# Optimization experiments

Hardware: AMD Instinct MI355X
Metric: run time of the kernel (lower is better)

Reference implementation:

```python
import jax, jax.numpy as jnp
import numpy as np

B, S, E, L = 4, 4096, 1024, 64
SCALE = float(np.sqrt(L))


def setup_inputs() -> dict:
    key = jax.random.key(0)
    ks = jax.random.split(key, 7)
    x = jax.random.normal(ks[0], (B, S, E), dtype=jnp.float32)
    # causal mask: positions with mask==0 are disallowed (masked_fill semantics)
    mask = jnp.tril(jnp.ones((S, S), dtype=jnp.int32))
    # Linear params (torch Linear: y = x @ W.T + b); store as [E, L] for x @ W
    sd = 1.0 / np.sqrt(E)
    Wq = jax.random.uniform(ks[1], (E, L), jnp.float32, -sd, sd)
    Wk = jax.random.uniform(ks[2], (E, L), jnp.float32, -sd, sd)
    Wv = jax.random.uniform(ks[3], (E, L), jnp.float32, -sd, sd)
    bq = jax.random.uniform(ks[4], (L,), jnp.float32, -sd, sd)
    bk = jax.random.uniform(ks[5], (L,), jnp.float32, -sd, sd)
    bv = jax.random.uniform(ks[6], (L,), jnp.float32, -sd, sd)
    return {"x": x, "Wq": Wq, "Wk": Wk, "Wv": Wv,
            "bq": bq, "bk": bk, "bv": bv, "mask": mask}


def reference(x, Wq, Wk, Wv, bq, bk, bv, mask):
    # Q,K,V: [B, S, L]
    Q = x @ Wq + bq
    K = x @ Wk + bk
    V = x @ Wv + bv
    # scores: [B, S, S] -- naive full matrix, faithful to the original
    scores = jnp.einsum('bsl,btl->bst', Q, K) / SCALE
    scores = jnp.where(mask == 0, -jnp.inf, scores)
    attn = jax.nn.softmax(scores, axis=-1)
    return jnp.einsum('bst,btl->bsl', attn, V)
```

## Files before the change

kernel.cpp:

```cpp
#include <hip/hip_runtime.h>
#include <hip/hip_bf16.h>
#include <cstdint>

typedef __bf16 bf16_t;
typedef __bf16 bf16x8 __attribute__((ext_vector_type(8)));
typedef float f32x4 __attribute__((ext_vector_type(4)));

#define B_ 4
#define S_ 4096
#define E_ 1024
#define L_ 64

__device__ __forceinline__ f32x4 mfma16(bf16x8 a, bf16x8 b, f32x4 c) {
  return __builtin_amdgcn_mfma_f32_16x16x32_bf16(a, b, c, 0, 0, 0);
}

template <int CTRL>
__device__ __forceinline__ float dpp_max_step(float x) {
  int t = __builtin_amdgcn_update_dpp(0, __float_as_int(x), CTRL, 0xF, 0xF, true);
  return fmaxf(x, __int_as_float(t));
}
template <int CTRL>
__device__ __forceinline__ float dpp_add_step(float x) {
  int t = __builtin_amdgcn_update_dpp(0, __float_as_int(x), CTRL, 0xF, 0xF, true);
  return x + __int_as_float(t);
}
__device__ __forceinline__ float dpp_reduce_max16(float x) {
  x = dpp_max_step<0x121>(x);
  x = dpp_max_step<0x122>(x);
  x = dpp_max_step<0x124>(x);
  x = dpp_max_step<0x128>(x);
  return x;
}
__device__ __forceinline__ float dpp_reduce_add16(float x) {
  x = dpp_add_step<0x121>(x);
  x = dpp_add_step<0x122>(x);
  x = dpp_add_step<0x124>(x);
  x = dpp_add_step<0x128>(x);
  return x;
}


__global__ void prep_w_kernel(const float* __restrict__ Wq, const float* __restrict__ Wk,
                              const float* __restrict__ Wv, bf16_t* __restrict__ Wf) {
  int n = blockIdx.x;
  const float* W = (n < 64) ? Wq : (n < 128 ? Wk : Wv);
  int col = n & 63;
  int nt = n >> 4, lr = n & 15;
  for (int k = threadIdx.x; k < E_; k += blockDim.x) {
    int kt = k >> 5, lg = (k >> 3) & 3, e = k & 7;
    Wf[((size_t)((nt * 32 + kt) * 64 + lg * 16 + lr) << 3) + e] = (bf16_t)W[(size_t)k * L_ + col];
  }
}

__global__ __launch_bounds__(512) void qkv_proj_kernel(
    const float* __restrict__ x, const bf16_t* __restrict__ Wf,
    const float* __restrict__ bq, const float* __restrict__ bk, const float* __restrict__ bv,
    bf16_t* __restrict__ Qf, bf16_t* __restrict__ Kf, bf16_t* __restrict__ Vf) {
  __shared__ __align__(16) char smem[32 * 1032 * 2];
  bf16_t* xls = reinterpret_cast<bf16_t*>(smem);
  bf16_t* stc = reinterpret_cast<bf16_t*>(smem);

  const int tid = threadIdx.x;
  const int w = tid >> 6, l = tid & 63;
  const int lr = l & 15, lg = l >> 4;
  const int rowgrp = w & 1, colgrp = w >> 1;
  const int m0 = blockIdx.x * 32;

  {
    const float* xb = x + (size_t)m0 * E_;
#pragma unroll
    for (int i = 0; i < 8; ++i) {
      const int base = (i * 512 + tid) * 8;
      float4 u0 = *reinterpret_cast<const float4*>(xb + base);
      float4 u1 = *reinterpret_cast<const float4*>(xb + base + 4);
      bf16x8 pk;
      pk[0] = (bf16_t)u0.x; pk[1] = (bf16_t)u0.y; pk[2] = (bf16_t)u0.z; pk[3] = (bf16_t)u0.w;
      pk[4] = (bf16_t)u1.x; pk[5] = (bf16_t)u1.y; pk[6] = (bf16_t)u1.z; pk[7] = (bf16_t)u1.w;
      const int row = base >> 10, col = base & 1023;
      *reinterpret_cast<bf16x8*>(xls + row * 1032 + col) = pk;
    }
  }
  __syncthreads();

  f32x4 acc[3];
#pragma unroll
  for (int t = 0; t < 3; ++t) acc[t] = f32x4{0.f, 0.f, 0.f, 0.f};

  const bf16_t* xa = xls + (size_t)(rowgrp * 16 + lr) * 1032 + lg * 8;
#pragma unroll
  for (int kt = 0; kt < 32; ++kt) {
    bf16x8 a = *reinterpret_cast<const bf16x8*>(xa + kt * 32);
#pragma unroll
    for (int t = 0; t < 3; ++t) {
      const int nt = colgrp * 3 + t;
      bf16x8 b = *reinterpret_cast<const bf16x8*>(Wf + (((size_t)(nt * 32 + kt) * 64 + l) << 3));
      acc[t] = mfma16(a, b, acc[t]);
    }
  }
  __syncthreads();

#pragma unroll
  for (int t = 0; t < 3; ++t) {
    const int colb = colgrp * 48 + t * 16;
    const int col = colb + lr;
    const int mat = colb >> 6;
    const float* bias = (mat == 0) ? bq : (mat == 1 ? bk : bv);
    const float bb = bias[col & 63];
#pragma unroll
    for (int r = 0; r < 4; ++r) {
      const int row = rowgrp * 16 + lg * 4 + r;
      stc[row * 200 + col] = (bf16_t)(acc[t][r] + bb);
    }
  }
  __syncthreads();

  if (tid < 256) {
    const int rt = tid >> 7, ktq = (tid >> 6) & 1, lane = tid & 63;
    const int lgw = lane >> 4, lrw = lane & 15;
    const int rtg = (m0 >> 4) + rt;
    bf16x8 qv = *reinterpret_cast<const bf16x8*>(stc + (rt * 16 + lrw) * 200 + ktq * 32 + lgw * 8);
    *reinterpret_cast<bf16x8*>(Qf + (((size_t)(rtg * 2 + ktq) * 64 + lane) << 3)) = qv;
    bf16x8 kv = *reinterpret_cast<const bf16x8*>(stc + (rt * 16 + lrw) * 200 + 64 + ktq * 32 + lgw * 8);
    *reinterpret_cast<bf16x8*>(Kf + (((size_t)(rtg * 2 + ktq) * 64 + lane) << 3)) = kv;
  } else {
    const int t2 = tid - 256;
    const int vt = t2 >> 6, lane = t2 & 63;
    const int lgv = lane >> 4, lrv = lane & 15;
    const int colv = vt * 16 + lrv;
    bf16x8 vv;
#pragma unroll
    for (int e = 0; e < 8; ++e)
      vv[e] = stc[(lgv * 8 + e) * 200 + 128 + colv];
    const int batch = m0 >> 12;
    const int stg = (m0 & (S_ - 1)) >> 5;
    *reinterpret_cast<bf16x8*>(Vf + ((size_t)batch << 18) + (((size_t)(stg * 4 + vt) * 64 + lane) << 3)) = vv;
  }
}

__global__ __launch_bounds__(256) void attn_kernel(
    const bf16_t* __restrict__ Qf, const bf16_t* __restrict__ Kf,
    const bf16_t* __restrict__ Vf, float* __restrict__ Opart, float* __restrict__ mlpart) {
  __shared__ __align__(16) bf16_t p_lds[4][16 * 72];
  __shared__ bf16_t od_lds[3][16][68];
  __shared__ float ml_lds[3][16][2];

  const int c = threadIdx.x >> 6, l = threadIdx.x & 63;
  const int lr = l & 15, lg = l >> 4;
  const int u = blockIdx.x;
  const int batch = u & 3;
  const int strip = (u >> 2) & 3;
  const int h = (u >> 4) & 1;
  const int qt = 63 - (u >> 5);
  const int qsi = ((u >> 5) << 4) | (u & 15);
  const int qrow = qt * 64 + strip * 16;
  const size_t qbase = (size_t)batch * S_ + qrow;
  bf16_t* pw = p_lds[c];

  const int rtq = batch * 256 + qt * 4 + strip;
  bf16x8 qa0 = *reinterpret_cast<const bf16x8*>(Qf + (((size_t)(rtq * 2) * 64 + l) << 3));
  bf16x8 qa1 = *reinterpret_cast<const bf16x8*>(Qf + (((size_t)(rtq * 2 + 1) * 64 + l) << 3));
  const bf16_t* Vb = Vf + ((size_t)batch << 18);

  f32x4 o[4];
  float m[4], ssum[4];
#pragma unroll
  for (int rr = 0; rr < 4; ++rr) { o[rr] = f32x4{0.f, 0.f, 0.f, 0.f}; m[rr] = -1e30f; ssum[rr] = 0.f; }

  for (int kt = 2 * c + h; kt <= qt; kt += 8) {
    const int t0 = kt * 64;
    f32x4 st[4];
#pragma unroll
    for (int cf = 0; cf < 4; ++cf) st[cf] = f32x4{0.f, 0.f, 0.f, 0.f};
#pragma unroll
    for (int cf = 0; cf < 4; ++cf) {
      const int rtk = batch * 256 + kt * 4 + cf;
      bf16x8 b0 = *reinterpret_cast<const bf16x8*>(Kf + (((size_t)(rtk * 2) * 64 + l) << 3));
      bf16x8 b1 = *reinterpret_cast<const bf16x8*>(Kf + (((size_t)(rtk * 2 + 1) * 64 + l) << 3));
      st[cf] = mfma16(qa0, b0, st[cf]);
      st[cf] = mfma16(qa1, b1, st[cf]);
    }
    const bool diag = (kt == qt);
    float p[4][4];
#pragma unroll
    for (int rr = 0; rr < 4; ++rr) {
      const int qg = qrow + lg * 4 + rr;
      float rowmax = -1e30f;
#pragma unroll
      for (int cf = 0; cf < 4; ++cf) {
        float s = st[cf][rr] * 0.125f;
        if (diag && (t0 + cf * 16 + lr) > qg) s = -1e30f;
        p[cf][rr] = s;
        rowmax = fmaxf(rowmax, s);
      }
      rowmax = dpp_reduce_max16(rowmax);
      float mnew = fmaxf(m[rr], rowmax);
      float scale = __expf(m[rr] - mnew);
      float rs = 0.f;
#pragma unroll
      for (int cf = 0; cf < 4; ++cf) {
        float e = __expf(p[cf][rr] - mnew);
        p[cf][rr] = e;
        rs += e;
      }
      rs = dpp_reduce_add16(rs);
      ssum[rr] = ssum[rr] * scale + rs;
#pragma unroll
      for (int cf = 0; cf < 4; ++cf) o[cf][rr] *= scale;
      m[rr] = mnew;
    }
#pragma unroll
    for (int rr = 0; rr < 4; ++rr)
#pragma unroll
      for (int cf = 0; cf < 4; ++cf)
        pw[(lg * 4 + rr) * 72 + cf * 16 + lr] = (bf16_t)p[cf][rr];
    bf16x8 pa0 = *reinterpret_cast<const bf16x8*>(pw + lr * 72 + lg * 8);
    bf16x8 pa1 = *reinterpret_cast<const bf16x8*>(pw + lr * 72 + 32 + lg * 8);
    const int st0 = kt * 2;
#pragma unroll
    for (int cf = 0; cf < 4; ++cf) {
      bf16x8 v0 = *reinterpret_cast<const bf16x8*>(Vb + (((size_t)((st0 * 4 + cf) * 64 + l)) << 3));
      bf16x8 v1 = *reinterpret_cast<const bf16x8*>(Vb + (((size_t)(((st0 + 1) * 4 + cf) * 64 + l)) << 3));
      o[cf] = mfma16(pa0, v0, o[cf]);
      o[cf] = mfma16(pa1, v1, o[cf]);
    }
  }

  if (c > 0) {
    if (lr == 0) {
#pragma unroll
      for (int rr = 0; rr < 4; ++rr) {
        ml_lds[c - 1][lg * 4 + rr][0] = m[rr];
        ml_lds[c - 1][lg * 4 + rr][1] = ssum[rr];
      }
    }
#pragma unroll
    for (int cf = 0; cf < 4; ++cf)
#pragma unroll
      for (int rr = 0; rr < 4; ++rr)
        od_lds[c - 1][lg * 4 + rr][cf * 16 + lr] = (bf16_t)o[cf][rr];
  }
  __syncthreads();
  if (c == 0) {
    float* Op = Opart + (size_t)(h * 1024 + qsi) * 1024;
    float* mlp = mlpart + (size_t)(h * 1024 + qsi) * 32;
#pragma unroll
    for (int rr = 0; rr < 4; ++rr) {
      const int row = lg * 4 + rr;
      float M = m[rr];
      float mv[3];
#pragma unroll
      for (int cc = 0; cc < 3; ++cc) {
        mv[cc] = ml_lds[cc][row][0];
        M = fmaxf(M, mv[cc]);
      }
      float f0 = __expf(m[rr] - M);
      float Lsum = ssum[rr] * f0;
      float fc[3];
#pragma unroll
      for (int cc = 0; cc < 3; ++cc) {
        fc[cc] = __expf(mv[cc] - M);
        Lsum += ml_lds[cc][row][1] * fc[cc];
      }
      if (lr == 0) { mlp[row * 2] = M; mlp[row * 2 + 1] = Lsum; }
#pragma unroll
      for (int cf = 0; cf < 4; ++cf) {
        float val = o[cf][rr] * f0;
#pragma unroll
        for (int cc = 0; cc < 3; ++cc)
          val += (float)od_lds[cc][row][cf * 16 + lr] * fc[cc];
        Op[row * 64 + cf * 16 + lr] = val;
      }
    }
  }
}

__global__ __launch_bounds__(64) void combine_kernel(
    const float* __restrict__ Opart, const float* __restrict__ mlpart,
    float* __restrict__ out) {
  const int b = blockIdx.x;
  const int batch = b & 3, strip = (b >> 2) & 3, qt = 63 - (b >> 4);
  const int l = threadIdx.x;
  const int row = l >> 2, c0 = (l & 3) * 16;
  const float* ml0 = mlpart + ((size_t)(0 * 1024 + b) * 16 + row) * 2;
  const float* ml1 = mlpart + ((size_t)(1 * 1024 + b) * 16 + row) * 2;
  float m0 = ml0[0], l0 = ml0[1], m1 = ml1[0], l1 = ml1[1];
  float M = fmaxf(m0, m1);
  float f0 = __expf(m0 - M), f1 = __expf(m1 - M);
  float inv = 1.f / (l0 * f0 + l1 * f1);
  const float* O0 = Opart + (size_t)(0 * 1024 + b) * 1024 + row * 64 + c0;
  const float* O1 = Opart + (size_t)(1 * 1024 + b) * 1024 + row * 64 + c0;
  float* dst = out + ((size_t)batch * S_ + qt * 64 + strip * 16 + row) * L_ + c0;
#pragma unroll
  for (int j = 0; j < 4; ++j) {
    float4 a = reinterpret_cast<const float4*>(O0)[j];
    float4 bb = reinterpret_cast<const float4*>(O1)[j];
    float4 v;
    v.x = (a.x * f0 + bb.x * f1) * inv;
    v.y = (a.y * f0 + bb.y * f1) * inv;
    v.z = (a.z * f0 + bb.z * f1) * inv;
    v.w = (a.w * f0 + bb.w * f1) * inv;
    reinterpret_cast<float4*>(dst)[j] = v;
  }
}

extern "C" void kernel_launch(void* const* d_in, const int* in_sizes, int n_in,
                              void* d_out, int out_size, void* d_ws, size_t ws_size,
                              hipStream_t stream) {
  (void)in_sizes; (void)n_in; (void)out_size; (void)ws_size;
  const float* x  = (const float*)d_in[0];
  const float* Wq = (const float*)d_in[1];
  const float* Wk = (const float*)d_in[2];
  const float* Wv = (const float*)d_in[3];
  const float* bq = (const float*)d_in[4];
  const float* bk = (const float*)d_in[5];
  const float* bv = (const float*)d_in[6];
  float* out = (float*)d_out;

  char* ws = (char*)d_ws;
  bf16_t* Qf  = (bf16_t*)(ws + 0);
  bf16_t* Kf  = (bf16_t*)(ws + (size_t)2 * 1024 * 1024);
  bf16_t* Vf  = (bf16_t*)(ws + (size_t)4 * 1024 * 1024);
  bf16_t* Wf  = (bf16_t*)(ws + (size_t)6 * 1024 * 1024);
  float* Opart = (float*)(ws + (size_t)7 * 1024 * 1024);
  float* mlpart = (float*)(ws + (size_t)15 * 1024 * 1024);

  hipLaunchKernelGGL(prep_w_kernel, dim3(192), dim3(256), 0, stream, Wq, Wk, Wv, Wf);
  hipLaunchKernelGGL(qkv_proj_kernel, dim3(16384 / 32), dim3(512), 0, stream,
                     x, Wf, bq, bk, bv, Qf, Kf, Vf);
  hipLaunchKernelGGL(attn_kernel, dim3(2048), dim3(256), 0, stream,
                     Qf, Kf, Vf, Opart, mlpart);
  hipLaunchKernelGGL(combine_kernel, dim3(1024), dim3(64), 0, stream,
                     Opart, mlpart, out);
}
```

Before: 61.48 us.

## Split QKV projection K-dimension in halves to overlap LDS staging with MFMA

Loads the whole 32x1024 x tile into registers at once, then converts and stores the two K-halves to separate LDS buffers. The MFMAs on the first half run while the second half is being written. Launch bounds add a minimum of 4 blocks per CU. The aim is to hide global-load and conversion latency in the projection kernel, at the cost of more register pressure and an extra barrier.

```diff
diff --git a/kernel.cpp b/kernel.cpp
--- a/kernel.cpp
+++ b/kernel.cpp
@@ -53,48 +53,80 @@
   }
 }
 
-__global__ __launch_bounds__(512) void qkv_proj_kernel(
+__global__ __launch_bounds__(512, 4) void qkv_proj_kernel(
     const float* __restrict__ x, const bf16_t* __restrict__ Wf,
     const float* __restrict__ bq, const float* __restrict__ bk, const float* __restrict__ bv,
     bf16_t* __restrict__ Qf, bf16_t* __restrict__ Kf, bf16_t* __restrict__ Vf) {
-  __shared__ __align__(16) char smem[32 * 1032 * 2];
-  bf16_t* xls = reinterpret_cast<bf16_t*>(smem);
-  bf16_t* stc = reinterpret_cast<bf16_t*>(smem);
+  __shared__ __align__(16) bf16_t xh[2][32][520];
+  bf16_t* stc = &xh[0][0][0];
 
   const int tid = threadIdx.x;
   const int w = tid >> 6, l = tid & 63;
   const int lr = l & 15, lg = l >> 4;
   const int rowgrp = w & 1, colgrp = w >> 1;
   const int m0 = blockIdx.x * 32;
-
-  {
-    const float* xb = x + (size_t)m0 * E_;
-#pragma unroll
-    for (int i = 0; i < 8; ++i) {
-      const int base = (i * 512 + tid) * 8;
-      float4 u0 = *reinterpret_cast<const float4*>(xb + base);
-      float4 u1 = *reinterpret_cast<const float4*>(xb + base + 4);
-      bf16x8 pk;
-      pk[0] = (bf16_t)u0.x; pk[1] = (bf16_t)u0.y; pk[2] = (bf16_t)u0.z; pk[3] = (bf16_t)u0.w;
-      pk[4] = (bf16_t)u1.x; pk[5] = (bf16_t)u1.y; pk[6] = (bf16_t)u1.z; pk[7] = (bf16_t)u1.w;
-      const int row = base >> 10, col = base & 1023;
-      *reinterpret_cast<bf16x8*>(xls + row * 1032 + col) = pk;
-    }
-  }
-  __syncthreads();
+  const float* xb = x + (size_t)m0 * E_;
+
+  float4 r0[8], r1[8];
+#pragma unroll
+  for (int i = 0; i < 4; ++i) {
+    const int gi = i * 512 + tid;
+    const int row = gi >> 6, col = (gi & 63) * 8;
+    const float* p0 = xb + (size_t)row * E_ + col;
+    r0[2 * i] = *reinterpret_cast<const float4*>(p0);
+    r0[2 * i + 1] = *reinterpret_cast<const float4*>(p0 + 4);
+    const float* p1 = p0 + 512;
+    r1[2 * i] = *reinterpret_cast<const float4*>(p1);
+    r1[2 * i + 1] = *reinterpret_cast<const float4*>(p1 + 4);
+  }
+#pragma unroll
+  for (int i = 0; i < 4; ++i) {
+    const int gi = i * 512 + tid;
+    const int row = gi >> 6, col = (gi & 63) * 8;
+    bf16x8 pk;
+    pk[0] = (bf16_t)r0[2 * i].x; pk[1] = (bf16_t)r0[2 * i].y;
+    pk[2] = (bf16_t)r0[2 * i].z; pk[3] = (bf16_t)r0[2 * i].w;
+    pk[4] = (bf16_t)r0[2 * i + 1].x; pk[5] = (bf16_t)r0[2 * i + 1].y;
+    pk[6] = (bf16_t)r0[2 * i + 1].z; pk[7] = (bf16_t)r0[2 * i + 1].w;
+    *reinterpret_cast<bf16x8*>(&xh[0][row][col]) = pk;
+  }
+  __syncthreads();
+#pragma unroll
+  for (int i = 0; i < 4; ++i) {
+    const int gi = i * 512 + tid;
+    const int row = gi >> 6, col = (gi & 63) * 8;
+    bf16x8 pk;
+    pk[0] = (bf16_t)r1[2 * i].x; pk[1] = (bf16_t)r1[2 * i].y;
+    pk[2] = (bf16_t)r1[2 * i].z; pk[3] = (bf16_t)r1[2 * i].w;
+    pk[4] = (bf16_t)r1[2 * i + 1].x; pk[5] = (bf16_t)r1[2 * i + 1].y;
+    pk[6] = (bf16_t)r1[2 * i + 1].z; pk[7] = (bf16_t)r1[2 * i + 1].w;
+    *reinterpret_cast<bf16x8*>(&xh[1][row][col]) = pk;
+  }
 
   f32x4 acc[3];
 #pragma unroll
   for (int t = 0; t < 3; ++t) acc[t] = f32x4{0.f, 0.f, 0.f, 0.f};
 
-  const bf16_t* xa = xls + (size_t)(rowgrp * 16 + lr) * 1032 + lg * 8;
-#pragma unroll
-  for (int kt = 0; kt < 32; ++kt) {
-    bf16x8 a = *reinterpret_cast<const bf16x8*>(xa + kt * 32);
+  const bf16_t* xa0 = &xh[0][rowgrp * 16 + lr][lg * 8];
+#pragma unroll
+  for (int kt2 = 0; kt2 < 16; ++kt2) {
+    bf16x8 a = *reinterpret_cast<const bf16x8*>(xa0 + kt2 * 32);
 #pragma unroll
     for (int t = 0; t < 3; ++t) {
       const int nt = colgrp * 3 + t;
-      bf16x8 b = *reinterpret_cast<const bf16x8*>(Wf + (((size_t)(nt * 32 + kt) * 64 + l) << 3));
+      bf16x8 b = *reinterpret_cast<const bf16x8*>(Wf + (((size_t)(nt * 32 + kt2) * 64 + l) << 3));
+      acc[t] = mfma16(a, b, acc[t]);
+    }
+  }
+  __syncthreads();
+  const bf16_t* xa1 = &xh[1][rowgrp * 16 + lr][lg * 8];
+#pragma unroll
+  for (int kt2 = 0; kt2 < 16; ++kt2) {
+    bf16x8 a = *reinterpret_cast<const bf16x8*>(xa1 + kt2 * 32);
+#pragma unroll
+    for (int t = 0; t < 3; ++t) {
+      const int nt = colgrp * 3 + t;
+      bf16x8 b = *reinterpret_cast<const bf16x8*>(Wf + (((size_t)(nt * 32 + 16 + kt2) * 64 + l) << 3));
       acc[t] = mfma16(a, b, acc[t]);
     }
   }
```

New measurement: 62.32 us. No clear change (+1.4%).

## Double-buffer x chunks in QKV projection with larger 64-row tiles

Applied to the files above, without the earlier changes.

Restructures the QKV projection kernel so each block handles 64 rows with 256 threads, streaming x in 128-column chunks through a double-buffered LDS region with register prefetch. Each wave now reuses its W fragments across four row tiles, cutting global W reads per output row. The full 32x1024 x staging of the old version is replaced by a software pipeline that overlaps global loads with MFMA work. The cost is more accumulator registers, fewer blocks (256), and a sync per chunk.

```diff
diff --git a/kernel.cpp b/kernel.cpp
--- a/kernel.cpp
+++ b/kernel.cpp
@@ -53,89 +53,124 @@
   }
 }
 
-__global__ __launch_bounds__(512) void qkv_proj_kernel(
+__global__ __launch_bounds__(256) void qkv_proj_kernel(
     const float* __restrict__ x, const bf16_t* __restrict__ Wf,
     const float* __restrict__ bq, const float* __restrict__ bk, const float* __restrict__ bv,
     bf16_t* __restrict__ Qf, bf16_t* __restrict__ Kf, bf16_t* __restrict__ Vf) {
-  __shared__ __align__(16) char smem[32 * 1032 * 2];
-  bf16_t* xls = reinterpret_cast<bf16_t*>(smem);
-  bf16_t* stc = reinterpret_cast<bf16_t*>(smem);
+  __shared__ __align__(16) bf16_t xbuf[2][64][136];
+  bf16_t* stc = &xbuf[0][0][0];
 
   const int tid = threadIdx.x;
   const int w = tid >> 6, l = tid & 63;
   const int lr = l & 15, lg = l >> 4;
-  const int rowgrp = w & 1, colgrp = w >> 1;
-  const int m0 = blockIdx.x * 32;
-
-  {
-    const float* xb = x + (size_t)m0 * E_;
-#pragma unroll
-    for (int i = 0; i < 8; ++i) {
-      const int base = (i * 512 + tid) * 8;
-      float4 u0 = *reinterpret_cast<const float4*>(xb + base);
-      float4 u1 = *reinterpret_cast<const float4*>(xb + base + 4);
-      bf16x8 pk;
-      pk[0] = (bf16_t)u0.x; pk[1] = (bf16_t)u0.y; pk[2] = (bf16_t)u0.z; pk[3] = (bf16_t)u0.w;
-      pk[4] = (bf16_t)u1.x; pk[5] = (bf16_t)u1.y; pk[6] = (bf16_t)u1.z; pk[7] = (bf16_t)u1.w;
-      const int row = base >> 10, col = base & 1023;
-      *reinterpret_cast<bf16x8*>(xls + row * 1032 + col) = pk;
-    }
-  }
+  const int cg = w;
+  const int m0 = blockIdx.x * 64;
+
+  float4 ra[4], rb[4];
+  const int g0 = tid;
+  int prow[4], pcol[4];
+#pragma unroll
+  for (int p = 0; p < 4; ++p) {
+    const int g = p * 256 + g0;
+    prow[p] = g >> 4;
+    pcol[p] = (g & 15) * 8;
+  }
+
+#define QKV_LOADREG(c)                                                        \
+  {                                                                           \
+    _Pragma("unroll") for (int p = 0; p < 4; ++p) {                           \
+      const float* src = x + (size_t)(m0 + prow[p]) * E_ + (c) * 128 + pcol[p]; \
+      ra[p] = *reinterpret_cast<const float4*>(src);                          \
+      rb[p] = *reinterpret_cast<const float4*>(src + 4);                      \
+    }                                                                         \
+  }
+#define QKV_WRITE(b)                                                          \
+  {                                                                           \
+    _Pragma("unroll") for (int p = 0; p < 4; ++p) {                           \
+      bf16x8 pk;                                                              \
+      pk[0] = (bf16_t)ra[p].x; pk[1] = (bf16_t)ra[p].y;                       \
+      pk[2] = (bf16_t)ra[p].z; pk[3] = (bf16_t)ra[p].w;                       \
+      pk[4] = (bf16_t)rb[p].x; pk[5] = (bf16_t)rb[p].y;                       \
+      pk[6] = (bf16_t)rb[p].z; pk[7] = (bf16_t)rb[p].w;                       \
+      *reinterpret_cast<bf16x8*>(&xbuf[(b)][prow[p]][pcol[p]]) = pk;          \
+    }                                                                         \
+  }
+
+  f32x4 acc[4][3];
+#pragma unroll
+  for (int rt = 0; rt < 4; ++rt)
+#pragma unroll
+    for (int t = 0; t < 3; ++t) acc[rt][t] = f32x4{0.f, 0.f, 0.f, 0.f};
+
+  QKV_LOADREG(0);
+  QKV_WRITE(0);
+  QKV_LOADREG(1);
   __syncthreads();
 
-  f32x4 acc[3];
-#pragma unroll
-  for (int t = 0; t < 3; ++t) acc[t] = f32x4{0.f, 0.f, 0.f, 0.f};
-
-  const bf16_t* xa = xls + (size_t)(rowgrp * 16 + lr) * 1032 + lg * 8;
-#pragma unroll
-  for (int kt = 0; kt < 32; ++kt) {
-    bf16x8 a = *reinterpret_cast<const bf16x8*>(xa + kt * 32);
-#pragma unroll
-    for (int t = 0; t < 3; ++t) {
-      const int nt = colgrp * 3 + t;
-      bf16x8 b = *reinterpret_cast<const bf16x8*>(Wf + (((size_t)(nt * 32 + kt) * 64 + l) << 3));
-      acc[t] = mfma16(a, b, acc[t]);
-    }
-  }
-  __syncthreads();
+  for (int c = 0; c < 8; ++c) {
+    const int cur = c & 1;
+#pragma unroll
+    for (int kt = 0; kt < 4; ++kt) {
+      const int ktg = c * 4 + kt;
+      bf16x8 bfr[3];
+#pragma unroll
+      for (int t = 0; t < 3; ++t) {
+        const int nt = cg * 3 + t;
+        bfr[t] = *reinterpret_cast<const bf16x8*>(Wf + (((size_t)(nt * 32 + ktg) * 64 + l) << 3));
+      }
+#pragma unroll
+      for (int rt = 0; rt < 4; ++rt) {
+        bf16x8 a = *reinterpret_cast<const bf16x8*>(&xbuf[cur][rt * 16 + lr][kt * 32 + lg * 8]);
+#pragma unroll
+        for (int t = 0; t < 3; ++t) acc[rt][t] = mfma16(a, bfr[t], acc[rt][t]);
+      }
+    }
+    if (c + 1 < 8) QKV_WRITE(cur ^ 1);
+    if (c + 2 < 8) QKV_LOADREG(c + 2);
+    __syncthreads();
+  }
 
 #pragma unroll
   for (int t = 0; t < 3; ++t) {
-    const int colb = colgrp * 48 + t * 16;
+    const int colb = cg * 48 + t * 16;
     const int col = colb + lr;
     const int mat = colb >> 6;
     const float* bias = (mat == 0) ? bq : (mat == 1 ? bk : bv);
     const float bb = bias[col & 63];
 #pragma unroll
-    for (int r = 0; r < 4; ++r) {
-      const int row = rowgrp * 16 + lg * 4 + r;
-      stc[row * 200 + col] = (bf16_t)(acc[t][r] + bb);
-    }
+    for (int rt = 0; rt < 4; ++rt)
+#pragma unroll
+      for (int r = 0; r < 4; ++r) {
+        const int row = rt * 16 + lg * 4 + r;
+        stc[row * 200 + col] = (bf16_t)(acc[rt][t][r] + bb);
+      }
   }
   __syncthreads();
 
-  if (tid < 256) {
-    const int rt = tid >> 7, ktq = (tid >> 6) & 1, lane = tid & 63;
+  {
+    const int lane = tid & 63;
     const int lgw = lane >> 4, lrw = lane & 15;
-    const int rtg = (m0 >> 4) + rt;
-    bf16x8 qv = *reinterpret_cast<const bf16x8*>(stc + (rt * 16 + lrw) * 200 + ktq * 32 + lgw * 8);
-    *reinterpret_cast<bf16x8*>(Qf + (((size_t)(rtg * 2 + ktq) * 64 + lane) << 3)) = qv;
-    bf16x8 kv = *reinterpret_cast<const bf16x8*>(stc + (rt * 16 + lrw) * 200 + 64 + ktq * 32 + lgw * 8);
-    *reinterpret_cast<bf16x8*>(Kf + (((size_t)(rtg * 2 + ktq) * 64 + lane) << 3)) = kv;
-  } else {
-    const int t2 = tid - 256;
-    const int vt = t2 >> 6, lane = t2 & 63;
-    const int lgv = lane >> 4, lrv = lane & 15;
-    const int colv = vt * 16 + lrv;
-    bf16x8 vv;
-#pragma unroll
-    for (int e = 0; e < 8; ++e)
-      vv[e] = stc[(lgv * 8 + e) * 200 + 128 + colv];
-    const int batch = m0 >> 12;
-    const int stg = (m0 & (S_ - 1)) >> 5;
-    *reinterpret_cast<bf16x8*>(Vf + ((size_t)batch << 18) + (((size_t)(stg * 4 + vt) * 64 + lane) << 3)) = vv;
-  }
+#pragma unroll
+    for (int ii = 0; ii < 2; ++ii) {
+      const int rt = ii * 2 + (tid >> 7), ktq = (tid >> 6) & 1;
+      const int rtg = (m0 >> 4) + rt;
+      bf16x8 qv = *reinterpret_cast<const bf16x8*>(stc + (rt * 16 + lrw) * 200 + ktq * 32 + lgw * 8);
+      *reinterpret_cast<bf16x8*>(Qf + (((size_t)(rtg * 2 + ktq) * 64 + lane) << 3)) = qv;
+      bf16x8 kv = *reinterpret_cast<const bf16x8*>(stc + (rt * 16 + lrw) * 200 + 64 + ktq * 32 + lgw * 8);
+      *reinterpret_cast<bf16x8*>(Kf + (((size_t)(rtg * 2 + ktq) * 64 + lane) << 3)) = kv;
+      const int stl = ii, vt = tid >> 6;
+      const int colv = vt * 16 + lrw;
+      bf16x8 vv;
+#pragma unroll
+      for (int e = 0; e < 8; ++e)
+        vv[e] = stc[(stl * 32 + lgw * 8 + e) * 200 + 128 + colv];
+      const int batch = m0 >> 12;
+      const int stg = ((m0 & (S_ - 1)) >> 5) + stl;
+      *reinterpret_cast<bf16x8*>(Vf + ((size_t)batch << 18) + (((size_t)(stg * 4 + vt) * 64 + lane) << 3)) = vv;
+    }
+  }
+#undef QKV_LOADREG
+#undef QKV_WRITE
 }
 
 __global__ __launch_bounds__(256) void attn_kernel(
@@ -326,7 +361,7 @@
   float* mlpart = (float*)(ws + (size_t)15 * 1024 * 1024);
 
   hipLaunchKernelGGL(prep_w_kernel, dim3(192), dim3(256), 0, stream, Wq, Wk, Wv, Wf);
-  hipLaunchKernelGGL(qkv_proj_kernel, dim3(16384 / 32), dim3(512), 0, stream,
+  hipLaunchKernelGGL(qkv_proj_kernel, dim3(16384 / 64), dim3(256), 0, stream,
                      x, Wf, bq, bk, bv, Qf, Kf, Vf);
   hipLaunchKernelGGL(attn_kernel, dim3(2048), dim3(256), 0, stream,
                      Qf, Kf, Vf, Opart, mlpart);
```

Measured after the change: 59.43 us. -3.3%, faster.
